# Kernel optimization log

Measured on AMD Instinct MI355X. Metric: run time of the kernel, lower is better.

Reference implementation:

```python
import jax, jax.numpy as jnp
import numpy as np
import math

B, N, D_MODEL, H, D_HEAD = 2, 2048, 1024, 16, 64
EPS = 1e-6

def setup_inputs() -> dict:
    key = jax.random.key(0)
    ks = jax.random.split(key, 6)
    s = 1.0 / math.sqrt(D_MODEL)
    return {
        "X": jax.random.normal(ks[0], (B, N, D_MODEL), dtype=jnp.float32),
        "Wq": jax.random.normal(ks[1], (D_MODEL, H * D_HEAD), dtype=jnp.float32) * s,
        "Wk": jax.random.normal(ks[2], (D_MODEL, H * D_HEAD), dtype=jnp.float32) * s,
        "Wv": jax.random.normal(ks[3], (D_MODEL, H * D_HEAD), dtype=jnp.float32) * s,
        "Wo": jax.random.normal(ks[4], (H * D_HEAD, D_MODEL), dtype=jnp.float32) * s,
        "bo": jnp.zeros((D_MODEL,), dtype=jnp.float32),
    }

def reference(X, Wq, Wk, Wv, Wo, bo):
    b, n, _ = X.shape
    # project and split heads -> [b, h, n, d_head]
    def heads(Y):
        return Y.reshape(b, n, H, D_HEAD).transpose(0, 2, 1, 3)
    Q = heads(X @ Wq)
    K = heads(X @ Wk)
    V = heads(X @ Wv)
    # per-head L2 normalization of Q and K
    Q = Q / (jnp.linalg.norm(Q, axis=-1, keepdims=True) + EPS)
    K = K / (jnp.linalg.norm(K, axis=-1, keepdims=True) + EPS)
    # scores [b, h, n, n]
    A = jnp.einsum("bhqd,bhkd->bhqk", Q, K) / math.sqrt(D_HEAD)
    causal = jnp.triu(jnp.ones((n, n), dtype=bool), k=1)
    A = jnp.where(causal, -jnp.inf, A)
    A = jax.nn.softmax(A, axis=-1)
    V_hat = jnp.einsum("bhqk,bhkd->bhqd", A, V)
    V_hat = V_hat.transpose(0, 2, 1, 3).reshape(b, n, H * D_HEAD)
    return V_hat @ Wo + bo
```

## Files before the change

kernel.cpp:

```cpp
#include <hip/hip_runtime.h>
#include <hip/hip_bf16.h>
#include <math.h>

#define BATCH 2
#define NSEQ  2048
#define DM    1024
#define NH    16
#define DH    64
#define EPS_N 1e-6f

typedef unsigned short u16;
typedef __attribute__((ext_vector_type(8))) short short8;
typedef __attribute__((ext_vector_type(8))) unsigned short u16x8;
typedef __attribute__((ext_vector_type(4))) unsigned short u16x4;
typedef __attribute__((ext_vector_type(4))) float f32x4;

__device__ __forceinline__ u16 f2bf(float x) {
  __hip_bfloat16 h = __float2bfloat16(x);
  return *reinterpret_cast<u16*>(&h);
}

__device__ __forceinline__ void gl_lds16(const u16* g, u16* lds_base) {
  __builtin_amdgcn_global_load_lds(
      (__attribute__((address_space(1))) void*)g,
      (__attribute__((address_space(3))) void*)lds_base, 16, 0, 0);
}

__global__ __launch_bounds__(256) void prep(
    const float* __restrict__ X,
    const float* __restrict__ w0, const float* __restrict__ w1,
    const float* __restrict__ w2, const float* __restrict__ w3,
    u16* __restrict__ Xb, u16* __restrict__ WT) {
  const int id = blockIdx.x, tid = threadIdx.x;
  if (id >= 1024) {
    size_t base = ((size_t)(id - 1024) * 256 + tid) * 8;
    float4 f0 = *(const float4*)&X[base];
    float4 f1 = *(const float4*)&X[base + 4];
    u16x8 v;
    v[0] = f2bf(f0.x); v[1] = f2bf(f0.y); v[2] = f2bf(f0.z); v[3] = f2bf(f0.w);
    v[4] = f2bf(f1.x); v[5] = f2bf(f1.y); v[6] = f2bf(f1.z); v[7] = f2bf(f1.w);
    *(u16x8*)&Xb[base] = v;
    return;
  }
  const int z = id >> 8, xy = id & 255, bx = xy & 15, by = xy >> 4;
  const float* in = (z == 0) ? w0 : (z == 1) ? w1 : (z == 2) ? w2 : w3;
  u16* o = WT + (size_t)z * DM * DM;
  __shared__ u16 T[64][65];
  const int n0 = bx * 64, k0 = by * 64;
  #pragma unroll
  for (int i = 0; i < 4; i++) {
    int c = tid + 256 * i, row = c >> 4, col4 = c & 15;
    float4 f = *(const float4*)&in[(size_t)(k0 + row) * DM + n0 + col4 * 4];
    T[row][col4 * 4 + 0] = f2bf(f.x);
    T[row][col4 * 4 + 1] = f2bf(f.y);
    T[row][col4 * 4 + 2] = f2bf(f.z);
    T[row][col4 * 4 + 3] = f2bf(f.w);
  }
  __syncthreads();
  #pragma unroll
  for (int i = 0; i < 2; i++) {
    int c = tid + 256 * i, row = c >> 3, col8 = c & 7;
    u16x8 v;
    #pragma unroll
    for (int e = 0; e < 8; e++) v[e] = T[col8 * 8 + e][row];
    *(u16x8*)&o[(size_t)(n0 + row) * DM + k0 + col8 * 8] = v;
  }
}

#define GEMM128_MAINLOOP(Aptr, Btptr)                                          \
  __shared__ u16 As[128 * 64];                                                 \
  __shared__ u16 Bs[128 * 64];                                                 \
  const int tid = threadIdx.x, w = tid >> 6, lane = tid & 63;                  \
  const int ml = lane & 15, quad = lane >> 4;                                  \
  const int m0 = blockIdx.y * 128, n0 = blockIdx.x * 128;                      \
  const int wm = w & 1, wn = w >> 1;                                           \
  const int srow = lane >> 3;                      \
  const int scol = ((lane & 7) ^ srow) * 8;         \
  f32x4 acc[4][4];                                                             \
  _Pragma("unroll") for (int mi = 0; mi < 4; mi++)                             \
    _Pragma("unroll") for (int ni = 0; ni < 4; ni++)                           \
      _Pragma("unroll") for (int e = 0; e < 4; e++) acc[mi][ni][e] = 0.f;      \
  for (int k0 = 0; k0 < DM; k0 += 64) {                                        \
    __syncthreads();                                                           \
    _Pragma("unroll") for (int L = 0; L < 4; L++) {                            \
      int I = w * 4 + L;                                                       \
      gl_lds16(Aptr  + (size_t)(m0 + I * 8 + srow) * DM + k0 + scol,           \
               As + I * 512);                                                  \
      gl_lds16(Btptr + (size_t)(n0 + I * 8 + srow) * DM + k0 + scol,           \
               Bs + I * 512);                                                  \
    }                                                                          \
    __syncthreads();                                                           \
    _Pragma("unroll") for (int kk = 0; kk < 64; kk += 32) {                    \
      const int kc = kk >> 3;                          \
      short8 am[4], bn[4];                                                     \
      _Pragma("unroll") for (int i = 0; i < 4; i++) {                          \
        int ra = wm * 64 + i * 16 + ml;                                        \
        int rb = wn * 64 + i * 16 + ml;                                        \
        am[i] = *(const short8*)&As[ra * 64 + (((quad + kc) ^ (ra & 7)) * 8)]; \
        bn[i] = *(const short8*)&Bs[rb * 64 + (((quad + kc) ^ (rb & 7)) * 8)]; \
      }                                                                        \
      _Pragma("unroll") for (int mi = 0; mi < 4; mi++)                         \
        _Pragma("unroll") for (int ni = 0; ni < 4; ni++)                       \
          acc[mi][ni] = __builtin_amdgcn_mfma_f32_16x16x32_bf16(               \
              am[mi], bn[ni], acc[mi][ni], 0, 0, 0);                           \
    }                                                                          \
  }

__global__ __launch_bounds__(256) void gemm_qkv128(
    const u16* __restrict__ Xb, const u16* __restrict__ WT,
    u16* __restrict__ Qo, u16* __restrict__ Ko, u16* __restrict__ Vt) {
  const u16* Bt = WT + (size_t)blockIdx.z * DM * DM;
  GEMM128_MAINLOOP(Xb, Bt)
  const int z = blockIdx.z;
  if (z < 2) {
    u16* OutQK = (z == 0) ? Qo : Ko;
    const float qsc = (z == 0) ? 0.125f : 1.0f;
    const int h = (n0 >> 6) + wn;
    #pragma unroll
    for (int mi = 0; mi < 4; mi++) {
      int mrow0 = m0 + wm * 64 + mi * 16 + quad * 4;
      int b = mrow0 >> 11, tok0 = mrow0 & (NSEQ - 1);
      #pragma unroll
      for (int r = 0; r < 4; r++) {
        float ss = 0.f;
        #pragma unroll
        for (int ni = 0; ni < 4; ni++) ss += acc[mi][ni][r] * acc[mi][ni][r];
        ss += __shfl_xor(ss, 1, 64);
        ss += __shfl_xor(ss, 2, 64);
        ss += __shfl_xor(ss, 4, 64);
        ss += __shfl_xor(ss, 8, 64);
        float sc = qsc / (sqrtf(ss) + EPS_N);
        #pragma unroll
        for (int ni = 0; ni < 4; ni++)
          OutQK[((size_t)(b * NH + h) * NSEQ + tok0 + r) * DH + ni * 16 + ml] =
              f2bf(acc[mi][ni][r] * sc);
      }
    }
  } else {
    #pragma unroll
    for (int mi = 0; mi < 4; mi++) {
      int mrow0 = m0 + wm * 64 + mi * 16 + quad * 4;
      int b = mrow0 >> 11, tok0 = mrow0 & (NSEQ - 1);
      #pragma unroll
      for (int ni = 0; ni < 4; ni++) {
        int n = n0 + wn * 64 + ni * 16 + ml;
        int h = n >> 6, d = n & 63;
        u16x4 pk;
        #pragma unroll
        for (int r = 0; r < 4; r++) pk[r] = f2bf(acc[mi][ni][r]);
        *(u16x4*)&Vt[((size_t)(b * NH + h) * DH + d) * NSEQ + tok0] = pk;
      }
    }
  }
}

__global__ __launch_bounds__(256) void gemm_proj128(
    const u16* __restrict__ A, const u16* __restrict__ BtW,
    const float* __restrict__ bias, float* __restrict__ out) {
  GEMM128_MAINLOOP(A, BtW)
  #pragma unroll
  for (int ni = 0; ni < 4; ni++) {
    int n = n0 + wn * 64 + ni * 16 + ml;
    float bz = bias[n];
    #pragma unroll
    for (int mi = 0; mi < 4; mi++) {
      int mrow0 = m0 + wm * 64 + mi * 16 + quad * 4;
      #pragma unroll
      for (int r = 0; r < 4; r++)
        out[(size_t)(mrow0 + r) * DM + n] = acc[mi][ni][r] + bz;
    }
  }
}

__global__ __launch_bounds__(256) void flash_attn(
    const u16* __restrict__ Qb, const u16* __restrict__ Kb,
    const u16* __restrict__ Vt, u16* __restrict__ vhat) {
  const int tid = threadIdx.x, w = tid >> 6, lane = tid & 63;
  const int ml = lane & 15, quad = lane >> 4;
  const int wq = w & 1, wk = w >> 1;
  const int bh = blockIdx.x;
  const int bb = bh >> 4, hb = bh & 15;
  const int pair = blockIdx.y;
  const u16* Qh = Qb + (size_t)bh * NSEQ * DH;
  const u16* Kh = Kb + (size_t)bh * NSEQ * DH;
  const u16* Vth = Vt + (size_t)bh * DH * NSEQ;

  __shared__ u16 Ks [64][72];
  __shared__ u16 VsT[64][72];
  __shared__ u16 Ps [4][16][40];
  __shared__ float Os[2][16][66];
  __shared__ float Ls[2][16];

  const int vd = tid >> 2, vc = tid & 3;

  for (int ph = 0; ph < 2; ph++) {
    const int qb32 = ph ? (63 - pair) : pair;
    const int q0 = qb32 * 32;
    const int ntiles = (qb32 >> 1) + 1;

    short8 aq[2];
    #pragma unroll
    for (int c = 0; c < 2; c++)
      aq[c] = *(const short8*)&Qh[(size_t)(q0 + wq * 16 + ml) * DH + c * 32 + quad * 8];

    f32x4 oacc[4];
    #pragma unroll
    for (int n = 0; n < 4; n++)
      #pragma unroll
      for (int e = 0; e < 4; e++) oacc[n][e] = 0.f;
    float l_[4] = {0.f, 0.f, 0.f, 0.f};

    for (int t = 0; t < ntiles; t++) {
      const int j0 = t * 64;
      u16x8 kreg[2], vreg[2];
      #pragma unroll
      for (int i = 0; i < 2; i++) {
        kreg[i] = *(const u16x8*)&Kh[(size_t)(j0 + lane) * DH + (w + 4 * i) * 8];
        vreg[i] = *(const u16x8*)&Vth[(size_t)vd * NSEQ + j0 + (vc + 4 * i) * 8];
      }
      __syncthreads();
      #pragma unroll
      for (int i = 0; i < 2; i++) {
        *(u16x8*)&Ks[lane][(w + 4 * i) * 8] = kreg[i];
        *(u16x8*)&VsT[vd][(vc + 4 * i) * 8] = vreg[i];
      }
      __syncthreads();

      f32x4 sacc[2];
      #pragma unroll
      for (int n = 0; n < 2; n++)
        #pragma unroll
        for (int e = 0; e < 4; e++) sacc[n][e] = 0.f;
      #pragma unroll
      for (int c = 0; c < 2; c++)
        #pragma unroll
        for (int n = 0; n < 2; n++) {
          short8 bf = *(const short8*)&Ks[wk * 32 + n * 16 + ml][c * 32 + quad * 8];
          sacc[n] = __builtin_amdgcn_mfma_f32_16x16x32_bf16(aq[c], bf, sacc[n], 0, 0, 0);
        }

      const bool lastt = (t == ntiles - 1);
      float p[2][4];
      #pragma unroll
      for (int n = 0; n < 2; n++) {
        int j = j0 + wk * 32 + n * 16 + ml;
        #pragma unroll
        for (int r = 0; r < 4; r++) {
          int q = q0 + wq * 16 + quad * 4 + r;
          float e = __expf(sacc[n][r]);
          p[n][r] = (lastt && j > q) ? 0.f : e;
          l_[r] += p[n][r];
        }
      }

      #pragma unroll
      for (int n = 0; n < 2; n++)
        #pragma unroll
        for (int r = 0; r < 4; r++)
          Ps[w][quad * 4 + r][n * 16 + ml] = f2bf(p[n][r]);

      short8 ap = *(const short8*)&Ps[w][ml][quad * 8];
      #pragma unroll
      for (int n = 0; n < 4; n++) {
        short8 bv = *(const short8*)&VsT[n * 16 + ml][wk * 32 + quad * 8];
        oacc[n] = __builtin_amdgcn_mfma_f32_16x16x32_bf16(ap, bv, oacc[n], 0, 0, 0);
      }
    }

    float lred[4];
    #pragma unroll
    for (int r = 0; r < 4; r++) {
      float lv = l_[r];
      lv += __shfl_xor(lv, 1, 64);
      lv += __shfl_xor(lv, 2, 64);
      lv += __shfl_xor(lv, 4, 64);
      lv += __shfl_xor(lv, 8, 64);
      lred[r] = lv;
    }
    if (wk == 0) {
      #pragma unroll
      for (int n = 0; n < 4; n++)
        #pragma unroll
        for (int r = 0; r < 4; r++)
          Os[wq][quad * 4 + r][n * 16 + ml] = oacc[n][r];
      if (ml == 0) {
        #pragma unroll
        for (int r = 0; r < 4; r++) Ls[wq][quad * 4 + r] = lred[r];
      }
    }
    __syncthreads();
    if (wk == 1) {
      #pragma unroll
      for (int r = 0; r < 4; r++) {
        float inv = 1.f / (lred[r] + Ls[wq][quad * 4 + r]);
        int q = q0 + wq * 16 + quad * 4 + r;
        #pragma unroll
        for (int n = 0; n < 4; n++) {
          float o = oacc[n][r] + Os[wq][quad * 4 + r][n * 16 + ml];
          vhat[((size_t)(bb * NSEQ + q)) * DM + hb * DH + n * 16 + ml] =
              f2bf(o * inv);
        }
      }
    }
  }
}

extern "C" void kernel_launch(void* const* d_in, const int* in_sizes, int n_in,
                              void* d_out, int out_size, void* d_ws, size_t ws_size,
                              hipStream_t stream) {
  const float* X  = (const float*)d_in[0];
  const float* Wq = (const float*)d_in[1];
  const float* Wk = (const float*)d_in[2];
  const float* Wv = (const float*)d_in[3];
  const float* Wo = (const float*)d_in[4];
  const float* bo = (const float*)d_in[5];
  float* out = (float*)d_out;

  const size_t NE = (size_t)BATCH * NSEQ * DM;
  u16* Qb   = (u16*)d_ws;
  u16* Kb   = Qb + NE;
  u16* Vt   = Kb + NE;
  u16* XbVh = Vt + NE;
  u16* WT   = XbVh + NE;

  prep        <<<dim3(3072),      256, 0, stream>>>(X, Wq, Wk, Wv, Wo, XbVh, WT);
  gemm_qkv128 <<<dim3(8, 32, 3),  256, 0, stream>>>(XbVh, WT, Qb, Kb, Vt);
  flash_attn  <<<dim3(32, 32),    256, 0, stream>>>(Qb, Kb, Vt, XbVh);
  gemm_proj128<<<dim3(8, 32, 1),  256, 0, stream>>>(XbVh, WT + 3 * (size_t)DM * DM,
                                                    bo, out);
}
```

Baseline: 203.9 us.

## Rewrite flash attention as single-wave blocks loading K/V fragments directly from global

Each attention block becomes one 64-thread wavefront that handles 32 query rows, with one block per query block instead of paired workloads. K and V fragments are read straight from global memory into registers, and K for the next step is prefetched, so the shared-memory staging, __syncthreads barriers and cross-wave output reduction go away. The cost is redundant global/L2 traffic for K/V, since each wave rereads them with no reuse across waves. Load balance now relies on many small blocks scheduled longest-first rather than pairing short and long rows.

```diff
diff --git a/kernel.cpp b/kernel.cpp
--- a/kernel.cpp
+++ b/kernel.cpp
@@ -172,137 +172,117 @@
   }
 }
 
-__global__ __launch_bounds__(256) void flash_attn(
+__global__ __launch_bounds__(64) void flash_attn(
     const u16* __restrict__ Qb, const u16* __restrict__ Kb,
     const u16* __restrict__ Vt, u16* __restrict__ vhat) {
-  const int tid = threadIdx.x, w = tid >> 6, lane = tid & 63;
+  const int lane = threadIdx.x;
   const int ml = lane & 15, quad = lane >> 4;
-  const int wq = w & 1, wk = w >> 1;
   const int bh = blockIdx.x;
   const int bb = bh >> 4, hb = bh & 15;
-  const int pair = blockIdx.y;
+  const int qblk = 63 - (int)blockIdx.y;
+  const int q0 = qblk * 32;
+  const int nsteps = qblk + 1;
   const u16* Qh = Qb + (size_t)bh * NSEQ * DH;
   const u16* Kh = Kb + (size_t)bh * NSEQ * DH;
   const u16* Vth = Vt + (size_t)bh * DH * NSEQ;
 
-  __shared__ u16 Ks [64][72];
-  __shared__ u16 VsT[64][72];
-  __shared__ u16 Ps [4][16][40];
-  __shared__ float Os[2][16][66];
-  __shared__ float Ls[2][16];
-
-  const int vd = tid >> 2, vc = tid & 3;
-
-  for (int ph = 0; ph < 2; ph++) {
-    const int qb32 = ph ? (63 - pair) : pair;
-    const int q0 = qb32 * 32;
-    const int ntiles = (qb32 >> 1) + 1;
-
-    short8 aq[2];
+  __shared__ u16 Ps[32][40];
+
+  short8 aq[2][2];
+  #pragma unroll
+  for (int m = 0; m < 2; m++)
     #pragma unroll
     for (int c = 0; c < 2; c++)
-      aq[c] = *(const short8*)&Qh[(size_t)(q0 + wq * 16 + ml) * DH + c * 32 + quad * 8];
-
-    f32x4 oacc[4];
+      aq[m][c] = *(const short8*)
+          &Qh[(size_t)(q0 + m * 16 + ml) * DH + c * 32 + quad * 8];
+
+  f32x4 oacc[2][4];
+  #pragma unroll
+  for (int m = 0; m < 2; m++)
     #pragma unroll
     for (int n = 0; n < 4; n++)
       #pragma unroll
-      for (int e = 0; e < 4; e++) oacc[n][e] = 0.f;
-    float l_[4] = {0.f, 0.f, 0.f, 0.f};
-
-    for (int t = 0; t < ntiles; t++) {
-      const int j0 = t * 64;
-      u16x8 kreg[2], vreg[2];
-      #pragma unroll
-      for (int i = 0; i < 2; i++) {
-        kreg[i] = *(const u16x8*)&Kh[(size_t)(j0 + lane) * DH + (w + 4 * i) * 8];
-        vreg[i] = *(const u16x8*)&Vth[(size_t)vd * NSEQ + j0 + (vc + 4 * i) * 8];
+      for (int e = 0; e < 4; e++) oacc[m][n][e] = 0.f;
+  float l_[2][4] = {{0.f, 0.f, 0.f, 0.f}, {0.f, 0.f, 0.f, 0.f}};
+
+  short8 kf[2][2];
+  #pragma unroll
+  for (int n = 0; n < 2; n++)
+    #pragma unroll
+    for (int c = 0; c < 2; c++)
+      kf[n][c] = *(const short8*)
+          &Kh[(size_t)(n * 16 + ml) * DH + c * 32 + quad * 8];
+
+  for (int s = 0; s < nsteps; s++) {
+    const int j0 = s * 32;
+    short8 vf[4];
+    #pragma unroll
+    for (int n = 0; n < 4; n++)
+      vf[n] = *(const short8*)&Vth[(size_t)(n * 16 + ml) * NSEQ + j0 + quad * 8];
+
+    f32x4 sacc[2][2];
+    #pragma unroll
+    for (int m = 0; m < 2; m++)
+      #pragma unroll
+      for (int n = 0; n < 2; n++) {
+        #pragma unroll
+        for (int e = 0; e < 4; e++) sacc[m][n][e] = 0.f;
+        #pragma unroll
+        for (int c = 0; c < 2; c++)
+          sacc[m][n] = __builtin_amdgcn_mfma_f32_16x16x32_bf16(
+              aq[m][c], kf[n][c], sacc[m][n], 0, 0, 0);
       }
-      __syncthreads();
-      #pragma unroll
-      for (int i = 0; i < 2; i++) {
-        *(u16x8*)&Ks[lane][(w + 4 * i) * 8] = kreg[i];
-        *(u16x8*)&VsT[vd][(vc + 4 * i) * 8] = vreg[i];
-      }
-      __syncthreads();
-
-      f32x4 sacc[2];
-      #pragma unroll
-      for (int n = 0; n < 2; n++)
-        #pragma unroll
-        for (int e = 0; e < 4; e++) sacc[n][e] = 0.f;
+
+    const int j0n = (j0 + 32 < NSEQ) ? (j0 + 32) : (NSEQ - 32);
+    #pragma unroll
+    for (int n = 0; n < 2; n++)
       #pragma unroll
       for (int c = 0; c < 2; c++)
-        #pragma unroll
-        for (int n = 0; n < 2; n++) {
-          short8 bf = *(const short8*)&Ks[wk * 32 + n * 16 + ml][c * 32 + quad * 8];
-          sacc[n] = __builtin_amdgcn_mfma_f32_16x16x32_bf16(aq[c], bf, sacc[n], 0, 0, 0);
-        }
-
-      const bool lastt = (t == ntiles - 1);
-      float p[2][4];
+        kf[n][c] = *(const short8*)
+            &Kh[(size_t)(j0n + n * 16 + ml) * DH + c * 32 + quad * 8];
+
+    const bool lastt = (s == nsteps - 1);
+    #pragma unroll
+    for (int m = 0; m < 2; m++)
       #pragma unroll
       for (int n = 0; n < 2; n++) {
-        int j = j0 + wk * 32 + n * 16 + ml;
+        int j = j0 + n * 16 + ml;
         #pragma unroll
         for (int r = 0; r < 4; r++) {
-          int q = q0 + wq * 16 + quad * 4 + r;
-          float e = __expf(sacc[n][r]);
-          p[n][r] = (lastt && j > q) ? 0.f : e;
-          l_[r] += p[n][r];
+          int q = q0 + m * 16 + quad * 4 + r;
+          float e = __expf(sacc[m][n][r]);
+          e = (lastt && j > q) ? 0.f : e;
+          l_[m][r] += e;
+          Ps[m * 16 + quad * 4 + r][n * 16 + ml] = f2bf(e);
         }
       }
 
-      #pragma unroll
-      for (int n = 0; n < 2; n++)
-        #pragma unroll
-        for (int r = 0; r < 4; r++)
-          Ps[w][quad * 4 + r][n * 16 + ml] = f2bf(p[n][r]);
-
-      short8 ap = *(const short8*)&Ps[w][ml][quad * 8];
-      #pragma unroll
-      for (int n = 0; n < 4; n++) {
-        short8 bv = *(const short8*)&VsT[n * 16 + ml][wk * 32 + quad * 8];
-        oacc[n] = __builtin_amdgcn_mfma_f32_16x16x32_bf16(ap, bv, oacc[n], 0, 0, 0);
-      }
-    }
-
-    float lred[4];
+    #pragma unroll
+    for (int m = 0; m < 2; m++) {
+      short8 ap = *(const short8*)&Ps[m * 16 + ml][quad * 8];
+      #pragma unroll
+      for (int n = 0; n < 4; n++)
+        oacc[m][n] = __builtin_amdgcn_mfma_f32_16x16x32_bf16(
+            ap, vf[n], oacc[m][n], 0, 0, 0);
+    }
+  }
+
+  #pragma unroll
+  for (int m = 0; m < 2; m++)
     #pragma unroll
     for (int r = 0; r < 4; r++) {
-      float lv = l_[r];
+      float lv = l_[m][r];
       lv += __shfl_xor(lv, 1, 64);
       lv += __shfl_xor(lv, 2, 64);
       lv += __shfl_xor(lv, 4, 64);
       lv += __shfl_xor(lv, 8, 64);
-      lred[r] = lv;
-    }
-    if (wk == 0) {
+      float inv = 1.f / lv;
+      int q = q0 + m * 16 + quad * 4 + r;
       #pragma unroll
       for (int n = 0; n < 4; n++)
-        #pragma unroll
-        for (int r = 0; r < 4; r++)
-          Os[wq][quad * 4 + r][n * 16 + ml] = oacc[n][r];
-      if (ml == 0) {
-        #pragma unroll
-        for (int r = 0; r < 4; r++) Ls[wq][quad * 4 + r] = lred[r];
-      }
-    }
-    __syncthreads();
-    if (wk == 1) {
-      #pragma unroll
-      for (int r = 0; r < 4; r++) {
-        float inv = 1.f / (lred[r] + Ls[wq][quad * 4 + r]);
-        int q = q0 + wq * 16 + quad * 4 + r;
-        #pragma unroll
-        for (int n = 0; n < 4; n++) {
-          float o = oacc[n][r] + Os[wq][quad * 4 + r][n * 16 + ml];
-          vhat[((size_t)(bb * NSEQ + q)) * DM + hb * DH + n * 16 + ml] =
-              f2bf(o * inv);
-        }
-      }
-    }
-  }
+        vhat[((size_t)(bb * NSEQ + q)) * DM + hb * DH + n * 16 + ml] =
+            f2bf(oacc[m][n][r] * inv);
+    }
 }
 
 extern "C" void kernel_launch(void* const* d_in, const int* in_sizes, int n_in,
@@ -325,7 +305,7 @@
 
   prep        <<<dim3(3072),      256, 0, stream>>>(X, Wq, Wk, Wv, Wo, XbVh, WT);
   gemm_qkv128 <<<dim3(8, 32, 3),  256, 0, stream>>>(XbVh, WT, Qb, Kb, Vt);
-  flash_attn  <<<dim3(32, 32),    256, 0, stream>>>(Qb, Kb, Vt, XbVh);
+  flash_attn  <<<dim3(32, 64),     64, 0, stream>>>(Qb, Kb, Vt, XbVh);
   gemm_proj128<<<dim3(8, 32, 1),  256, 0, stream>>>(XbVh, WT + 3 * (size_t)DM * DM,
                                                     bo, out);
 }
```

Result: slower. 224.3 us (+10.0%).
